# Performance work log

Hardware: AMD Instinct MI355X
Metric: run time of the kernel (lower is better)

Reference implementation:

```python
import jax, jax.numpy as jnp
import numpy as np

NV, NC, E = 100000, 50000, 800000
VD, CD, H, ROUNDS = 4, 1, 128, 2


def _ln(x, g, b):
    mu = jnp.mean(x, axis=-1, keepdims=True)
    v = jnp.mean((x - mu) ** 2, axis=-1, keepdims=True)
    return (x - mu) * jax.lax.rsqrt(v + 1e-5) * g + b


def _agg(msg, dst, n):
    # degree-normalized scatter-add: out[v] = sum_{e: dst[e]=v} msg[e] / (deg(v)+1e-6)
    s = jax.ops.segment_sum(msg, dst, num_segments=n)
    cnt = jax.ops.segment_sum(jnp.ones((msg.shape[0],), msg.dtype), dst, num_segments=n)
    return s / (cnt[:, None] + 1e-6)


def setup_inputs() -> dict:
    key = jax.random.key(0)
    ks = jax.random.split(key, 16)
    p = lambda k, sh: jax.random.normal(k, sh, jnp.float32) * 0.05
    z = lambda: jnp.zeros((H,), jnp.float32)
    o = lambda: jnp.ones((H,), jnp.float32)
    return {
        'x_var': jax.random.normal(ks[0], (NV, VD), jnp.float32),
        'x_con': jax.random.normal(ks[1], (NC, CD), jnp.float32),
        'e_vc_src': jax.random.randint(ks[2], (E,), 0, NV, jnp.int32),
        'e_vc_dst': jax.random.randint(ks[3], (E,), 0, NC, jnp.int32),
        'e_cv_src': jax.random.randint(ks[4], (E,), 0, NC, jnp.int32),
        'e_cv_dst': jax.random.randint(ks[5], (E,), 0, NV, jnp.int32),
        'var_proj_w': p(ks[6], (VD, H)), 'var_proj_b': z(),
        'con_proj_w': p(ks[7], (CD, H)), 'con_proj_b': z(),
        'v2c_msg_w': p(ks[8], (H, H)), 'v2c_msg_b': z(),
        'v2c_upd_w': p(ks[9], (H + 1, H)), 'v2c_upd_b': z(),
        'v2c_ln_g': o(), 'v2c_ln_b': z(),
        'c2v_msg_w': p(ks[10], (H, H)), 'c2v_msg_b': z(),
        'c2v_ln_g': o(), 'c2v_ln_b': z(),
        'var_gate_w': p(ks[11], (2 * H, H)), 'var_gate_b': z(),
        'con_gate_w': p(ks[12], (2 * H, H)), 'con_gate_b': z(),
        'var_ln_g': o(), 'var_ln_b': z(),
        'con_ln_g': o(), 'con_ln_b': z(),
    }


def reference(x_var, x_con, e_vc_src, e_vc_dst, e_cv_src, e_cv_dst,
              var_proj_w, var_proj_b, con_proj_w, con_proj_b,
              v2c_msg_w, v2c_msg_b, v2c_upd_w, v2c_upd_b, v2c_ln_g, v2c_ln_b,
              c2v_msg_w, c2v_msg_b, c2v_ln_g, c2v_ln_b,
              var_gate_w, var_gate_b, con_gate_w, con_gate_b,
              var_ln_g, var_ln_b, con_ln_g, con_ln_b):
    clue = x_con[:, 0]  # (NC,)
    hv = _ln(jax.nn.relu(x_var @ var_proj_w + var_proj_b), var_ln_g, var_ln_b)  # (NV,H)
    hc = _ln(jax.nn.relu(x_con @ con_proj_w + con_proj_b), con_ln_g, con_ln_b)  # (NC,H)
    for _ in range(ROUNDS):
        # var -> con
        msg = hv[e_vc_src] @ v2c_msg_w + v2c_msg_b  # (E,H)
        agg = _agg(msg, e_vc_dst, NC)
        upd = jnp.concatenate([agg, clue[:, None]], axis=1)  # (NC,H+1)
        con_new = _ln(jax.nn.relu(upd @ v2c_upd_w + v2c_upd_b), v2c_ln_g, v2c_ln_b)
        g = jax.nn.sigmoid(jnp.concatenate([hc, con_new], axis=1) @ con_gate_w + con_gate_b)
        hc = g * con_new + (1 - g) * hc
        # con -> var
        msg2 = hc[e_cv_src] @ c2v_msg_w + c2v_msg_b  # (E,H)
        var_new = _ln(jax.nn.relu(_agg(msg2, e_cv_dst, NV)), c2v_ln_g, c2v_ln_b)
        g2 = jax.nn.sigmoid(jnp.concatenate([hv, var_new], axis=1) @ var_gate_w + var_gate_b)
        hv = g2 * var_new + (1 - g2) * hv
    return hv
```

## Files before the change

### kernel.cpp

```cpp
#include <hip/hip_runtime.h>
#include <stdint.h>

#define NVN 100000
#define NCN 50000
#define NE  800000
#define H   128

typedef __attribute__((ext_vector_type(8))) short bf16x8;
typedef __attribute__((ext_vector_type(4))) float f32x4;

static __device__ __forceinline__ float wredsum(float v) {
#pragma unroll
  for (int off = 32; off > 0; off >>= 1) v += __shfl_xor(v, off, 64);
  return v;
}
static __device__ __forceinline__ float sigmoidf(float x) { return 1.0f / (1.0f + __expf(-x)); }
static __device__ __forceinline__ unsigned short f2bf(float f) {
  unsigned int u = __float_as_uint(f);
  return (unsigned short)((u + 0x7FFFu + ((u >> 16) & 1u)) >> 16);
}
static __device__ __forceinline__ short2 splitbf(float f) {
  unsigned short h = f2bf(f);
  float hf = __uint_as_float(((unsigned int)h) << 16);
  short2 r;
  r.x = (short)h;
  r.y = (short)f2bf(f - hf);
  return r;
}

__global__ __launch_bounds__(256) void k_init_var(const float* __restrict__ xv,
    const float* __restrict__ w, const float* __restrict__ b,
    const float* __restrict__ g, const float* __restrict__ bb,
    float* __restrict__ hv, unsigned short* __restrict__ hb) {
  int wid = (blockIdx.x * 256 + threadIdx.x) >> 6;
  int lane = threadIdx.x & 63;
  if (wid >= NVN) return;
  float x0 = xv[wid*4+0], x1 = xv[wid*4+1], x2 = xv[wid*4+2], x3 = xv[wid*4+3];
  int c0 = lane, c1 = lane + 64;
  float v0 = b[c0] + x0*w[c0] + x1*w[H+c0] + x2*w[2*H+c0] + x3*w[3*H+c0];
  float v1 = b[c1] + x0*w[c1] + x1*w[H+c1] + x2*w[2*H+c1] + x3*w[3*H+c1];
  v0 = fmaxf(v0, 0.f); v1 = fmaxf(v1, 0.f);
  float mu = wredsum(v0 + v1) * (1.0f/H);
  float d0 = v0 - mu, d1 = v1 - mu;
  float var = wredsum(d0*d0 + d1*d1) * (1.0f/H);
  float r = rsqrtf(var + 1e-5f);
  float o0 = d0*r*g[c0] + bb[c0], o1 = d1*r*g[c1] + bb[c1];
  hv[(size_t)wid*H + c0] = o0;  hv[(size_t)wid*H + c1] = o1;
  hb[(size_t)wid*H + c0] = f2bf(o0);  hb[(size_t)wid*H + c1] = f2bf(o1);
}

__global__ __launch_bounds__(256) void k_init_con(const float* __restrict__ xc,
    const float* __restrict__ w, const float* __restrict__ b,
    const float* __restrict__ g, const float* __restrict__ bb,
    float* __restrict__ hc, unsigned short* __restrict__ hb) {
  int wid = (blockIdx.x * 256 + threadIdx.x) >> 6;
  int lane = threadIdx.x & 63;
  if (wid >= NCN) return;
  float x = xc[wid];
  int c0 = lane, c1 = lane + 64;
  float v0 = fmaxf(b[c0] + x*w[c0], 0.f);
  float v1 = fmaxf(b[c1] + x*w[c1], 0.f);
  float mu = wredsum(v0 + v1) * (1.0f/H);
  float d0 = v0 - mu, d1 = v1 - mu;
  float var = wredsum(d0*d0 + d1*d1) * (1.0f/H);
  float r = rsqrtf(var + 1e-5f);
  float o0 = d0*r*g[c0] + bb[c0], o1 = d1*r*g[c1] + bb[c1];
  hc[(size_t)wid*H + c0] = o0;  hc[(size_t)wid*H + c1] = o1;
  hb[(size_t)wid*H + c0] = f2bf(o0);  hb[(size_t)wid*H + c1] = f2bf(o1);
}

__global__ void k_fuse_w(const float* __restrict__ wm, const float* __restrict__ wu,
                         float* __restrict__ wf) {
  int idx = blockIdx.x*256 + threadIdx.x;
  int i = idx >> 7, j = idx & 127;
  float a = 0.f;
  for (int k = 0; k < H; ++k) a = fmaf(wm[i*H+k], wu[k*H+j], a);
  wf[idx] = a;
}
__global__ void k_fuse_b(const float* __restrict__ bm, const float* __restrict__ wu,
                         float* __restrict__ bf) {
  int j = threadIdx.x;
  float a = 0.f;
  for (int k = 0; k < H; ++k) a = fmaf(bm[k], wu[k*H+j], a);
  bf[j] = a;
}

__global__ __launch_bounds__(256) void k_perm2(const float* __restrict__ W,
    unsigned short* __restrict__ Whi, unsigned short* __restrict__ Wlo, int K) {
  int idx = blockIdx.x*256 + threadIdx.x;
  if (idx >= K*H) return;
  int j = idx & 7, lane = (idx >> 3) & 63, ct = (idx >> 9) & 7, kb = idx >> 12;
  int k = kb*32 + (lane >> 4)*8 + j, c = ct*16 + (lane & 15);
  float w = W[k*H + c];
  unsigned short h = f2bf(w);
  float hf = __uint_as_float(((unsigned int)h) << 16);
  Whi[idx] = h;
  Wlo[idx] = f2bf(w - hf);
}

__global__ void k_count(const int* __restrict__ dc, const int* __restrict__ dv,
                        int* __restrict__ cnt_c, int* __restrict__ cnt_v) {
  for (int e = blockIdx.x*blockDim.x + threadIdx.x; e < NE; e += gridDim.x*blockDim.x) {
    atomicAdd(&cnt_c[dc[e]], 1);
    atomicAdd(&cnt_v[dv[e]], 1);
  }
}
__global__ __launch_bounds__(256) void k_scan1m(
    const int* __restrict__ in_c, int* __restrict__ out_c, int* __restrict__ aux_c, int nbc, int n_c,
    const int* __restrict__ in_v, int* __restrict__ out_v, int* __restrict__ aux_v, int n_v) {
  const int b = blockIdx.x;
  const int* in; int* out; int* aux; int n; int lb;
  if (b < nbc) { in = in_c; out = out_c; aux = aux_c; n = n_c; lb = b; }
  else         { in = in_v; out = out_v; aux = aux_v; n = n_v; lb = b - nbc; }
  __shared__ int s[256];
  int t = threadIdx.x, i = lb*256 + t;
  int v = (i < n) ? in[i] : 0;
  s[t] = v; __syncthreads();
  for (int off = 1; off < 256; off <<= 1) {
    int x = (t >= off) ? s[t - off] : 0;
    __syncthreads();
    s[t] += x;
    __syncthreads();
  }
  if (i < n) out[i] = s[t] - v;
  if (t == 255) aux[lb] = s[255];
}
__global__ __launch_bounds__(1024) void k_scan2m(int* __restrict__ aux_c, int nbc,
                                                 int* __restrict__ aux_v, int nbv) {
  int* aux = (blockIdx.x == 0) ? aux_c : aux_v;
  int nb   = (blockIdx.x == 0) ? nbc : nbv;
  __shared__ int s[1024];
  int t = threadIdx.x;
  int v = (t < nb) ? aux[t] : 0;
  s[t] = v; __syncthreads();
  for (int off = 1; off < 1024; off <<= 1) {
    int x = (t >= off) ? s[t-off] : 0;
    __syncthreads();
    s[t] += x;
    __syncthreads();
  }
  if (t < nb) aux[t] = s[t] - v;
}
__global__ __launch_bounds__(256) void k_scan3m(
    int* __restrict__ out_c, const int* __restrict__ aux_c, int nbc, int n_c,
    int* __restrict__ out_v, const int* __restrict__ aux_v, int n_v, int total) {
  const int b = blockIdx.x;
  int* out; const int* aux; int n; int lb;
  if (b < nbc) { out = out_c; aux = aux_c; n = n_c; lb = b; }
  else         { out = out_v; aux = aux_v; n = n_v; lb = b - nbc; }
  int i = lb*256 + threadIdx.x;
  if (i < n) out[i] += aux[lb];
  if (i == 0) out[n] = total;
}
__global__ void k_scatter(const int* __restrict__ sc, const int* __restrict__ dc,
                          const int* __restrict__ sv, const int* __restrict__ dv,
                          const int* __restrict__ off_c, int* __restrict__ cur_c, int* __restrict__ lst_c,
                          const int* __restrict__ off_v, int* __restrict__ cur_v, int* __restrict__ lst_v) {
  for (int e = blockIdx.x*blockDim.x + threadIdx.x; e < NE; e += gridDim.x*blockDim.x) {
    int d = dc[e]; int p = atomicAdd(&cur_c[d], 1); lst_c[off_c[d] + p] = sc[e];
    d = dv[e];     p = atomicAdd(&cur_v[d], 1);     lst_v[off_v[d] + p] = sv[e];
  }
}

__global__ __launch_bounds__(256) void k_gather_bf(const unsigned int* __restrict__ tab,
    const int* __restrict__ off, const int* __restrict__ lst,
    float* __restrict__ out, int n) {
  int wid = (blockIdx.x * 256 + threadIdx.x) >> 6;
  int lane = threadIdx.x & 63;
  if (wid >= n) return;
  int s0 = off[wid], s1 = off[wid+1];
  const int grp = lane >> 4, c16 = lane & 15;
  float acc[8];
#pragma unroll
  for (int j = 0; j < 8; ++j) acc[j] = 0.f;
#pragma unroll 2
  for (int p = s0 + grp; p < s1; p += 4) {
    int idx = lst[p];
    uint4 u = *(const uint4*)(tab + (size_t)idx*64 + c16*4);
    acc[0] += __uint_as_float(u.x << 16);
    acc[1] += __uint_as_float(u.x & 0xFFFF0000u);
    acc[2] += __uint_as_float(u.y << 16);
    acc[3] += __uint_as_float(u.y & 0xFFFF0000u);
    acc[4] += __uint_as_float(u.z << 16);
    acc[5] += __uint_as_float(u.z & 0xFFFF0000u);
    acc[6] += __uint_as_float(u.w << 16);
    acc[7] += __uint_as_float(u.w & 0xFFFF0000u);
  }
#pragma unroll
  for (int j = 0; j < 8; ++j) {
    acc[j] += __shfl_xor(acc[j], 16, 64);
    acc[j] += __shfl_xor(acc[j], 32, 64);
  }
  if (lane < 16) {
    float inv = 1.0f / ((float)(s1 - s0) + 1e-6f);
    float* op = out + (size_t)wid*H + c16*8;
    *(float4*)(op)     = make_float4(acc[0]*inv, acc[1]*inv, acc[2]*inv, acc[3]*inv);
    *(float4*)(op + 4) = make_float4(acc[4]*inv, acc[5]*inv, acc[6]*inv, acc[7]*inv);
  }
}

template<int EPI>
__global__ __launch_bounds__(128) void k_mleg(
    const float* __restrict__ A,
    const unsigned short* __restrict__ Wph, const unsigned short* __restrict__ Wpl,
    const int* __restrict__ off, const float* __restrict__ xc,
    const float* __restrict__ vb, const float* __restrict__ wcl,
    const float* __restrict__ badd, const float* __restrict__ lng,
    const float* __restrict__ lnb,
    const unsigned short* __restrict__ Gph, const float* __restrict__ gb,
    float* __restrict__ Hm, unsigned short* __restrict__ Hb, int n) {
  __shared__ float lds[32][132];
  const int wv = threadIdx.x >> 6, lane = threadIdx.x & 63;
  const int rbase = blockIdx.x*32 + wv*16;
  if (rbase >= n) return;
  const int g = lane >> 4, c15 = lane & 15;
  int arow = rbase + c15; if (arow > n-1) arow = n-1;

  const float* Ar1 = Hm + (size_t)arow*H + g*8;
  float4 pf[8];
#pragma unroll
  for (int kb = 0; kb < 4; ++kb) {
    pf[2*kb]   = *(const float4*)(Ar1 + kb*32);
    pf[2*kb+1] = *(const float4*)(Ar1 + kb*32 + 4);
  }

  {
    const float* Ar = A + (size_t)arow*H + g*8;
    bf16x8 ahi[4], alo[4];
#pragma unroll
    for (int kb = 0; kb < 4; ++kb) {
      float4 p0 = *(const float4*)(Ar + kb*32);
      float4 p1 = *(const float4*)(Ar + kb*32 + 4);
      bf16x8 h, l;
      short2 s;
      s = splitbf(p0.x); h[0] = s.x; l[0] = s.y;
      s = splitbf(p0.y); h[1] = s.x; l[1] = s.y;
      s = splitbf(p0.z); h[2] = s.x; l[2] = s.y;
      s = splitbf(p0.w); h[3] = s.x; l[3] = s.y;
      s = splitbf(p1.x); h[4] = s.x; l[4] = s.y;
      s = splitbf(p1.y); h[5] = s.x; l[5] = s.y;
      s = splitbf(p1.z); h[6] = s.x; l[6] = s.y;
      s = splitbf(p1.w); h[7] = s.x; l[7] = s.y;
      ahi[kb] = h; alo[kb] = l;
    }
    const bf16x8* Bph = (const bf16x8*)Wph;
    const bf16x8* Bpl = (const bf16x8*)Wpl;
    f32x4 zero = {0.f, 0.f, 0.f, 0.f};
    f32x4 acc[8];
#pragma unroll
    for (int ct = 0; ct < 8; ++ct) acc[ct] = zero;
#pragma unroll
    for (int kb = 0; kb < 4; ++kb)
#pragma unroll
      for (int ct = 0; ct < 8; ++ct) {
        bf16x8 bh = Bph[(kb*8+ct)*64 + lane];
        bf16x8 bl = Bpl[(kb*8+ct)*64 + lane];
        acc[ct] = __builtin_amdgcn_mfma_f32_16x16x32_bf16(ahi[kb], bh, acc[ct], 0, 0, 0);
        acc[ct] = __builtin_amdgcn_mfma_f32_16x16x32_bf16(alo[kb], bh, acc[ct], 0, 0, 0);
        acc[ct] = __builtin_amdgcn_mfma_f32_16x16x32_bf16(ahi[kb], bl, acc[ct], 0, 0, 0);
      }
#pragma unroll
    for (int r = 0; r < 4; ++r)
#pragma unroll
      for (int ct = 0; ct < 8; ++ct)
        lds[wv*16 + g*4 + r][ct*16 + c15] = acc[ct][r];
  }

  {
    float vb0 = vb[lane], vb1 = vb[lane+64];
    float lg0 = lng[lane], lg1 = lng[lane+64];
    float lb0 = lnb[lane], lb1 = lnb[lane+64];
    float wc0 = 0.f, wc1 = 0.f, ba0 = 0.f, ba1 = 0.f;
    if constexpr (EPI == 0) {
      wc0 = wcl[lane]; wc1 = wcl[lane+64];
      ba0 = badd[lane]; ba1 = badd[lane+64];
    }
    auto lnrow = [&](int row, int dst) {
      float cf = (float)(off[dst+1] - off[dst]);
      float scale = cf / (cf + 1e-6f);
      float v0 = lds[row][lane]     + scale*vb0;
      float v1 = lds[row][lane+64]  + scale*vb1;
      if constexpr (EPI == 0) {
        float clue = xc[dst];
        v0 += clue*wc0 + ba0;
        v1 += clue*wc1 + ba1;
      }
      v0 = fmaxf(v0, 0.f); v1 = fmaxf(v1, 0.f);
      float mu = wredsum(v0 + v1) * (1.0f/H);
      float d0 = v0 - mu, d1 = v1 - mu;
      float var = wredsum(d0*d0 + d1*d1) * (1.0f/H);
      float r = rsqrtf(var + 1e-5f);
      lds[row][lane]      = d0*r*lg0 + lb0;
      lds[row][lane + 64] = d1*r*lg1 + lb1;
    };
    const int blk = blockIdx.x*32;
    if (blk + 32 <= n) {
#pragma unroll
      for (int i = 0; i < 16; ++i) lnrow(wv*16 + i, blk + wv*16 + i);
    } else {
      for (int i = 0; i < 16; ++i) {
        int dst = blk + wv*16 + i;
        if (dst >= n) break;
        lnrow(wv*16 + i, dst);
      }
    }
  }

  {
    bf16x8 ahi[8], alo[8];
#pragma unroll
    for (int kb = 0; kb < 4; ++kb) {
      float4 p0 = pf[2*kb];
      float4 p1 = pf[2*kb+1];
      bf16x8 h, l;
      short2 s;
      s = splitbf(p0.x); h[0] = s.x; l[0] = s.y;
      s = splitbf(p0.y); h[1] = s.x; l[1] = s.y;
      s = splitbf(p0.z); h[2] = s.x; l[2] = s.y;
      s = splitbf(p0.w); h[3] = s.x; l[3] = s.y;
      s = splitbf(p1.x); h[4] = s.x; l[4] = s.y;
      s = splitbf(p1.y); h[5] = s.x; l[5] = s.y;
      s = splitbf(p1.z); h[6] = s.x; l[6] = s.y;
      s = splitbf(p1.w); h[7] = s.x; l[7] = s.y;
      ahi[kb] = h; alo[kb] = l;
    }
    const float* Ar2 = &lds[wv*16 + c15][0];
#pragma unroll
    for (int kb = 4; kb < 8; ++kb) {
      float4 p0 = *(const float4*)(Ar2 + (kb-4)*32 + g*8);
      float4 p1 = *(const float4*)(Ar2 + (kb-4)*32 + g*8 + 4);
      bf16x8 h, l;
      short2 s;
      s = splitbf(p0.x); h[0] = s.x; l[0] = s.y;
      s = splitbf(p0.y); h[1] = s.x; l[1] = s.y;
      s = splitbf(p0.z); h[2] = s.x; l[2] = s.y;
      s = splitbf(p0.w); h[3] = s.x; l[3] = s.y;
      s = splitbf(p1.x); h[4] = s.x; l[4] = s.y;
      s = splitbf(p1.y); h[5] = s.x; l[5] = s.y;
      s = splitbf(p1.z); h[6] = s.x; l[6] = s.y;
      s = splitbf(p1.w); h[7] = s.x; l[7] = s.y;
      ahi[kb] = h; alo[kb] = l;
    }
    const bf16x8* Bph = (const bf16x8*)Gph;
    f32x4 zero = {0.f, 0.f, 0.f, 0.f};
    f32x4 acc[8];
#pragma unroll
    for (int ct = 0; ct < 8; ++ct) acc[ct] = zero;
#pragma unroll
    for (int kb = 0; kb < 8; ++kb)
#pragma unroll
      for (int ct = 0; ct < 8; ++ct) {
        bf16x8 bh = Bph[(kb*8+ct)*64 + lane];
        acc[ct] = __builtin_amdgcn_mfma_f32_16x16x32_bf16(ahi[kb], bh, acc[ct], 0, 0, 0);
        acc[ct] = __builtin_amdgcn_mfma_f32_16x16x32_bf16(alo[kb], bh, acc[ct], 0, 0, 0);
      }
    float gbv[8];
#pragma unroll
    for (int ct = 0; ct < 8; ++ct) gbv[ct] = gb[ct*16 + c15];
#pragma unroll
    for (int r = 0; r < 4; ++r) {
      int rg = rbase + g*4 + r;
      if (rg >= n) continue;
      int row = wv*16 + g*4 + r;
      float* hp = Hm + (size_t)rg*H + c15;
      unsigned short* hbp = Hb + (size_t)rg*H + c15;
#pragma unroll
      for (int ct = 0; ct < 8; ++ct) {
        float gg = sigmoidf(acc[ct][r] + gbv[ct]);
        float nv = lds[row][ct*16 + c15];
        float ov = hp[ct*16];
        float res = gg*nv + (1.f - gg)*ov;
        hp[ct*16] = res;
        hbp[ct*16] = f2bf(res);
      }
    }
  }
}

extern "C" void kernel_launch(void* const* d_in, const int* in_sizes, int n_in,
                              void* d_out, int out_size, void* d_ws, size_t ws_size,
                              hipStream_t stream) {
  const float* x_var   = (const float*)d_in[0];
  const float* x_con   = (const float*)d_in[1];
  const int*   evc_src = (const int*)d_in[2];
  const int*   evc_dst = (const int*)d_in[3];
  const int*   ecv_src = (const int*)d_in[4];
  const int*   ecv_dst = (const int*)d_in[5];
  const float* vproj_w = (const float*)d_in[6];
  const float* vproj_b = (const float*)d_in[7];
  const float* cproj_w = (const float*)d_in[8];
  const float* cproj_b = (const float*)d_in[9];
  const float* wmsg    = (const float*)d_in[10];
  const float* bmsg    = (const float*)d_in[11];
  const float* wupd    = (const float*)d_in[12];
  const float* bupd    = (const float*)d_in[13];
  const float* v2c_ln_g = (const float*)d_in[14];
  const float* v2c_ln_b = (const float*)d_in[15];
  const float* wc2v    = (const float*)d_in[16];
  const float* bc2v    = (const float*)d_in[17];
  const float* c2v_ln_g = (const float*)d_in[18];
  const float* c2v_ln_b = (const float*)d_in[19];
  const float* vgate_w = (const float*)d_in[20];
  const float* vgate_b = (const float*)d_in[21];
  const float* cgate_w = (const float*)d_in[22];
  const float* cgate_b = (const float*)d_in[23];
  const float* var_ln_g = (const float*)d_in[24];
  const float* var_ln_b = (const float*)d_in[25];
  const float* con_ln_g = (const float*)d_in[26];
  const float* con_ln_b = (const float*)d_in[27];
  float* hv = (float*)d_out;

  char* p = (char*)d_ws;
  auto carve = [&](size_t bytes) { char* r = p; p += (bytes + 255) & ~(size_t)255; return r; };
  int* cnt_c = (int*)carve((size_t)NCN*4);
  int* cur_c = (int*)carve((size_t)NCN*4);
  int* cnt_v = (int*)carve((size_t)NVN*4);
  int* cur_v = (int*)carve((size_t)NVN*4);
  int* off_c = (int*)carve((size_t)(NCN+1)*4);
  int* off_v = (int*)carve((size_t)(NVN+1)*4);
  int* aux_c = (int*)carve(1024*4);
  int* aux_v = (int*)carve(1024*4);
  int* lst_c = (int*)carve((size_t)NE*4);
  int* lst_v = (int*)carve((size_t)NE*4);
  float* wf  = (float*)carve((size_t)H*H*4);
  float* bfu = (float*)carve((size_t)H*4);
  unsigned short* wfph = (unsigned short*)carve((size_t)H*H*2);
  unsigned short* wfpl = (unsigned short*)carve((size_t)H*H*2);
  unsigned short* wvph = (unsigned short*)carve((size_t)H*H*2);
  unsigned short* wvpl = (unsigned short*)carve((size_t)H*H*2);
  unsigned short* cgph = (unsigned short*)carve((size_t)2*H*H*2);
  unsigned short* cgpl = (unsigned short*)carve((size_t)2*H*H*2);
  unsigned short* vgph = (unsigned short*)carve((size_t)2*H*H*2);
  unsigned short* vgpl = (unsigned short*)carve((size_t)2*H*H*2);
  float* hc    = (float*)carve((size_t)NCN*H*4);
  float* t_c   = (float*)carve((size_t)NCN*H*4);
  float* t_v   = (float*)carve((size_t)NVN*H*4);
  unsigned short* hvb = (unsigned short*)carve((size_t)NVN*H*2);
  unsigned short* hcb = (unsigned short*)carve((size_t)NCN*H*2);
  if ((size_t)(p - (char*)d_ws) > ws_size) return;

  (void)hipMemsetAsync(cnt_c, 0, (size_t)NCN*4, stream);
  (void)hipMemsetAsync(cur_c, 0, (size_t)NCN*4, stream);
  (void)hipMemsetAsync(cnt_v, 0, (size_t)NVN*4, stream);
  (void)hipMemsetAsync(cur_v, 0, (size_t)NVN*4, stream);

  k_fuse_w<<<64, 256, 0, stream>>>(wmsg, wupd, wf);
  k_fuse_b<<<1, 128, 0, stream>>>(bmsg, wupd, bfu);
  k_perm2<<<(H*H+255)/256, 256, 0, stream>>>(wf, wfph, wfpl, H);
  k_perm2<<<(H*H+255)/256, 256, 0, stream>>>(wc2v, wvph, wvpl, H);
  k_perm2<<<(2*H*H+255)/256, 256, 0, stream>>>(cgate_w, cgph, cgpl, 2*H);
  k_perm2<<<(2*H*H+255)/256, 256, 0, stream>>>(vgate_w, vgph, vgpl, 2*H);

  k_count<<<2048, 256, 0, stream>>>(evc_dst, ecv_dst, cnt_c, cnt_v);
  int nbc = (NCN + 255)/256, nbv = (NVN + 255)/256;
  k_scan1m<<<nbc + nbv, 256, 0, stream>>>(cnt_c, off_c, aux_c, nbc, NCN,
                                          cnt_v, off_v, aux_v, NVN);
  k_scan2m<<<2, 1024, 0, stream>>>(aux_c, nbc, aux_v, nbv);
  k_scan3m<<<nbc + nbv, 256, 0, stream>>>(off_c, aux_c, nbc, NCN,
                                          off_v, aux_v, NVN, NE);
  k_scatter<<<2048, 256, 0, stream>>>(evc_src, evc_dst, ecv_src, ecv_dst,
                                      off_c, cur_c, lst_c, off_v, cur_v, lst_v);

  k_init_var<<<NVN/4, 256, 0, stream>>>(x_var, vproj_w, vproj_b, var_ln_g, var_ln_b, hv, hvb);
  k_init_con<<<NCN/4, 256, 0, stream>>>(x_con, cproj_w, cproj_b, con_ln_g, con_ln_b, hc, hcb);

  for (int r = 0; r < 2; ++r) {
    k_gather_bf<<<(NCN+3)/4, 256, 0, stream>>>((const unsigned int*)hvb, off_c, lst_c, t_c, NCN);
    k_mleg<0><<<(NCN+31)/32, 128, 0, stream>>>(t_c, wfph, wfpl, off_c, x_con, bfu, wupd + H*H,
                                               bupd, v2c_ln_g, v2c_ln_b, cgph, cgate_b,
                                               hc, hcb, NCN);
    k_gather_bf<<<(NVN+3)/4, 256, 0, stream>>>((const unsigned int*)hcb, off_v, lst_v, t_v, NVN);
    k_mleg<1><<<(NVN+31)/32, 128, 0, stream>>>(t_v, wvph, wvpl, off_v, nullptr, bc2v, nullptr,
                                               nullptr, c2v_ln_g, c2v_ln_b, vgph, vgate_b,
                                               hv, hvb, NVN);
  }
}
```

Measured before the change: 588.6 us.

## Keep node states only in bf16, dropping fp32 state copies and the split gate MFMA

Node hidden states are now stored only as bf16 between rounds. The fp32 hv/hc buffers are no longer written by the init kernels and no longer read or written per round, except for the final fp32 output write. The old-state half of the gate GEMM uses the bf16 state directly in a single MFMA instead of hi/lo split pairs, which halves those MFMAs and removes the fp32 loads. This cuts memory traffic and compute, at the cost of accuracy, because the gated residual now mixes in a bf16-rounded old state.

```diff
diff --git a/kernel.cpp b/kernel.cpp
--- a/kernel.cpp
+++ b/kernel.cpp
@@ -19,9 +19,12 @@
   unsigned int u = __float_as_uint(f);
   return (unsigned short)((u + 0x7FFFu + ((u >> 16) & 1u)) >> 16);
 }
+static __device__ __forceinline__ float bf2f(unsigned short u) {
+  return __uint_as_float(((unsigned int)u) << 16);
+}
 static __device__ __forceinline__ short2 splitbf(float f) {
   unsigned short h = f2bf(f);
-  float hf = __uint_as_float(((unsigned int)h) << 16);
+  float hf = bf2f(h);
   short2 r;
   r.x = (short)h;
   r.y = (short)f2bf(f - hf);
@@ -31,7 +34,7 @@
 __global__ __launch_bounds__(256) void k_init_var(const float* __restrict__ xv,
     const float* __restrict__ w, const float* __restrict__ b,
     const float* __restrict__ g, const float* __restrict__ bb,
-    float* __restrict__ hv, unsigned short* __restrict__ hb) {
+    unsigned short* __restrict__ hb) {
   int wid = (blockIdx.x * 256 + threadIdx.x) >> 6;
   int lane = threadIdx.x & 63;
   if (wid >= NVN) return;
@@ -45,14 +48,13 @@
   float var = wredsum(d0*d0 + d1*d1) * (1.0f/H);
   float r = rsqrtf(var + 1e-5f);
   float o0 = d0*r*g[c0] + bb[c0], o1 = d1*r*g[c1] + bb[c1];
-  hv[(size_t)wid*H + c0] = o0;  hv[(size_t)wid*H + c1] = o1;
   hb[(size_t)wid*H + c0] = f2bf(o0);  hb[(size_t)wid*H + c1] = f2bf(o1);
 }
 
 __global__ __launch_bounds__(256) void k_init_con(const float* __restrict__ xc,
     const float* __restrict__ w, const float* __restrict__ b,
     const float* __restrict__ g, const float* __restrict__ bb,
-    float* __restrict__ hc, unsigned short* __restrict__ hb) {
+    unsigned short* __restrict__ hb) {
   int wid = (blockIdx.x * 256 + threadIdx.x) >> 6;
   int lane = threadIdx.x & 63;
   if (wid >= NCN) return;
@@ -65,7 +67,6 @@
   float var = wredsum(d0*d0 + d1*d1) * (1.0f/H);
   float r = rsqrtf(var + 1e-5f);
   float o0 = d0*r*g[c0] + bb[c0], o1 = d1*r*g[c1] + bb[c1];
-  hc[(size_t)wid*H + c0] = o0;  hc[(size_t)wid*H + c1] = o1;
   hb[(size_t)wid*H + c0] = f2bf(o0);  hb[(size_t)wid*H + c1] = f2bf(o1);
 }
 
@@ -93,9 +94,8 @@
   int k = kb*32 + (lane >> 4)*8 + j, c = ct*16 + (lane & 15);
   float w = W[k*H + c];
   unsigned short h = f2bf(w);
-  float hf = __uint_as_float(((unsigned int)h) << 16);
   Whi[idx] = h;
-  Wlo[idx] = f2bf(w - hf);
+  Wlo[idx] = f2bf(w - bf2f(h));
 }
 
 __global__ void k_count(const int* __restrict__ dc, const int* __restrict__ dv,
@@ -199,7 +199,7 @@
   }
 }
 
-template<int EPI>
+template<int EPI, int WRITEF>
 __global__ __launch_bounds__(128) void k_mleg(
     const float* __restrict__ A,
     const unsigned short* __restrict__ Wph, const unsigned short* __restrict__ Wpl,
@@ -208,7 +208,7 @@
     const float* __restrict__ badd, const float* __restrict__ lng,
     const float* __restrict__ lnb,
     const unsigned short* __restrict__ Gph, const float* __restrict__ gb,
-    float* __restrict__ Hm, unsigned short* __restrict__ Hb, int n) {
+    unsigned short* __restrict__ Hb, float* __restrict__ HmOut, int n) {
   __shared__ float lds[32][132];
   const int wv = threadIdx.x >> 6, lane = threadIdx.x & 63;
   const int rbase = blockIdx.x*32 + wv*16;
@@ -216,13 +216,10 @@
   const int g = lane >> 4, c15 = lane & 15;
   int arow = rbase + c15; if (arow > n-1) arow = n-1;
 
-  const float* Ar1 = Hm + (size_t)arow*H + g*8;
-  float4 pf[8];
-#pragma unroll
-  for (int kb = 0; kb < 4; ++kb) {
-    pf[2*kb]   = *(const float4*)(Ar1 + kb*32);
-    pf[2*kb+1] = *(const float4*)(Ar1 + kb*32 + 4);
-  }
+  const unsigned short* Hbr = Hb + (size_t)arow*H + g*8;
+  bf16x8 a1[4];
+#pragma unroll
+  for (int kb = 0; kb < 4; ++kb) a1[kb] = *(const bf16x8*)(Hbr + kb*32);
 
   {
     const float* Ar = A + (size_t)arow*H + g*8;
@@ -307,11 +304,12 @@
   }
 
   {
-    bf16x8 ahi[8], alo[8];
-#pragma unroll
-    for (int kb = 0; kb < 4; ++kb) {
-      float4 p0 = pf[2*kb];
-      float4 p1 = pf[2*kb+1];
+    bf16x8 chi[4], clo[4];
+    const float* Ar2 = &lds[wv*16 + c15][0];
+#pragma unroll
+    for (int i = 0; i < 4; ++i) {
+      float4 p0 = *(const float4*)(Ar2 + i*32 + g*8);
+      float4 p1 = *(const float4*)(Ar2 + i*32 + g*8 + 4);
       bf16x8 h, l;
       short2 s;
       s = splitbf(p0.x); h[0] = s.x; l[0] = s.y;
@@ -322,24 +320,7 @@
       s = splitbf(p1.y); h[5] = s.x; l[5] = s.y;
       s = splitbf(p1.z); h[6] = s.x; l[6] = s.y;
       s = splitbf(p1.w); h[7] = s.x; l[7] = s.y;
-      ahi[kb] = h; alo[kb] = l;
-    }
-    const float* Ar2 = &lds[wv*16 + c15][0];
-#pragma unroll
-    for (int kb = 4; kb < 8; ++kb) {
-      float4 p0 = *(const float4*)(Ar2 + (kb-4)*32 + g*8);
-      float4 p1 = *(const float4*)(Ar2 + (kb-4)*32 + g*8 + 4);
-      bf16x8 h, l;
-      short2 s;
-      s = splitbf(p0.x); h[0] = s.x; l[0] = s.y;
-      s = splitbf(p0.y); h[1] = s.x; l[1] = s.y;
-      s = splitbf(p0.z); h[2] = s.x; l[2] = s.y;
-      s = splitbf(p0.w); h[3] = s.x; l[3] = s.y;
-      s = splitbf(p1.x); h[4] = s.x; l[4] = s.y;
-      s = splitbf(p1.y); h[5] = s.x; l[5] = s.y;
-      s = splitbf(p1.z); h[6] = s.x; l[6] = s.y;
-      s = splitbf(p1.w); h[7] = s.x; l[7] = s.y;
-      ahi[kb] = h; alo[kb] = l;
+      chi[i] = h; clo[i] = l;
     }
     const bf16x8* Bph = (const bf16x8*)Gph;
     f32x4 zero = {0.f, 0.f, 0.f, 0.f};
@@ -347,12 +328,17 @@
 #pragma unroll
     for (int ct = 0; ct < 8; ++ct) acc[ct] = zero;
 #pragma unroll
-    for (int kb = 0; kb < 8; ++kb)
+    for (int kb = 0; kb < 4; ++kb)
+#pragma unroll
+      for (int ct = 0; ct < 8; ++ct)
+        acc[ct] = __builtin_amdgcn_mfma_f32_16x16x32_bf16(a1[kb], Bph[(kb*8+ct)*64 + lane], acc[ct], 0, 0, 0);
+#pragma unroll
+    for (int kb = 4; kb < 8; ++kb)
 #pragma unroll
       for (int ct = 0; ct < 8; ++ct) {
         bf16x8 bh = Bph[(kb*8+ct)*64 + lane];
-        acc[ct] = __builtin_amdgcn_mfma_f32_16x16x32_bf16(ahi[kb], bh, acc[ct], 0, 0, 0);
-        acc[ct] = __builtin_amdgcn_mfma_f32_16x16x32_bf16(alo[kb], bh, acc[ct], 0, 0, 0);
+        acc[ct] = __builtin_amdgcn_mfma_f32_16x16x32_bf16(chi[kb-4], bh, acc[ct], 0, 0, 0);
+        acc[ct] = __builtin_amdgcn_mfma_f32_16x16x32_bf16(clo[kb-4], bh, acc[ct], 0, 0, 0);
       }
     float gbv[8];
 #pragma unroll
@@ -362,16 +348,16 @@
       int rg = rbase + g*4 + r;
       if (rg >= n) continue;
       int row = wv*16 + g*4 + r;
-      float* hp = Hm + (size_t)rg*H + c15;
       unsigned short* hbp = Hb + (size_t)rg*H + c15;
+      float* hop = HmOut + (size_t)rg*H + c15;
 #pragma unroll
       for (int ct = 0; ct < 8; ++ct) {
         float gg = sigmoidf(acc[ct][r] + gbv[ct]);
         float nv = lds[row][ct*16 + c15];
-        float ov = hp[ct*16];
+        float ov = bf2f(hbp[ct*16]);
         float res = gg*nv + (1.f - gg)*ov;
-        hp[ct*16] = res;
         hbp[ct*16] = f2bf(res);
+        if constexpr (WRITEF) hop[ct*16] = res;
       }
     }
   }
@@ -432,7 +418,6 @@
   unsigned short* cgpl = (unsigned short*)carve((size_t)2*H*H*2);
   unsigned short* vgph = (unsigned short*)carve((size_t)2*H*H*2);
   unsigned short* vgpl = (unsigned short*)carve((size_t)2*H*H*2);
-  float* hc    = (float*)carve((size_t)NCN*H*4);
   float* t_c   = (float*)carve((size_t)NCN*H*4);
   float* t_v   = (float*)carve((size_t)NVN*H*4);
   unsigned short* hvb = (unsigned short*)carve((size_t)NVN*H*2);
@@ -461,17 +446,23 @@
   k_scatter<<<2048, 256, 0, stream>>>(evc_src, evc_dst, ecv_src, ecv_dst,
                                       off_c, cur_c, lst_c, off_v, cur_v, lst_v);
 
-  k_init_var<<<NVN/4, 256, 0, stream>>>(x_var, vproj_w, vproj_b, var_ln_g, var_ln_b, hv, hvb);
-  k_init_con<<<NCN/4, 256, 0, stream>>>(x_con, cproj_w, cproj_b, con_ln_g, con_ln_b, hc, hcb);
-
-  for (int r = 0; r < 2; ++r) {
-    k_gather_bf<<<(NCN+3)/4, 256, 0, stream>>>((const unsigned int*)hvb, off_c, lst_c, t_c, NCN);
-    k_mleg<0><<<(NCN+31)/32, 128, 0, stream>>>(t_c, wfph, wfpl, off_c, x_con, bfu, wupd + H*H,
+  k_init_var<<<NVN/4, 256, 0, stream>>>(x_var, vproj_w, vproj_b, var_ln_g, var_ln_b, hvb);
+  k_init_con<<<NCN/4, 256, 0, stream>>>(x_con, cproj_w, cproj_b, con_ln_g, con_ln_b, hcb);
+
+  k_gather_bf<<<(NCN+3)/4, 256, 0, stream>>>((const unsigned int*)hvb, off_c, lst_c, t_c, NCN);
+  k_mleg<0,0><<<(NCN+31)/32, 128, 0, stream>>>(t_c, wfph, wfpl, off_c, x_con, bfu, wupd + H*H,
                                                bupd, v2c_ln_g, v2c_ln_b, cgph, cgate_b,
-                                               hc, hcb, NCN);
-    k_gather_bf<<<(NVN+3)/4, 256, 0, stream>>>((const unsigned int*)hcb, off_v, lst_v, t_v, NVN);
-    k_mleg<1><<<(NVN+31)/32, 128, 0, stream>>>(t_v, wvph, wvpl, off_v, nullptr, bc2v, nullptr,
+                                               hcb, hv, NCN);
+  k_gather_bf<<<(NVN+3)/4, 256, 0, stream>>>((const unsigned int*)hcb, off_v, lst_v, t_v, NVN);
+  k_mleg<1,0><<<(NVN+31)/32, 128, 0, stream>>>(t_v, wvph, wvpl, off_v, nullptr, bc2v, nullptr,
                                                nullptr, c2v_ln_g, c2v_ln_b, vgph, vgate_b,
-                                               hv, hvb, NVN);
-  }
-}
+                                               hvb, hv, NVN);
+  k_gather_bf<<<(NCN+3)/4, 256, 0, stream>>>((const unsigned int*)hvb, off_c, lst_c, t_c, NCN);
+  k_mleg<0,0><<<(NCN+31)/32, 128, 0, stream>>>(t_c, wfph, wfpl, off_c, x_con, bfu, wupd + H*H,
+                                               bupd, v2c_ln_g, v2c_ln_b, cgph, cgate_b,
+                                               hcb, hv, NCN);
+  k_gather_bf<<<(NVN+3)/4, 256, 0, stream>>>((const unsigned int*)hcb, off_v, lst_v, t_v, NVN);
+  k_mleg<1,1><<<(NVN+31)/32, 128, 0, stream>>>(t_v, wvph, wvpl, off_v, nullptr, bc2v, nullptr,
+                                               nullptr, c2v_ln_g, c2v_ln_b, vgph, vgate_b,
+                                               hvb, hv, NVN);
+}
```

New measurement: 583.2 us. About the same (-0.9%).
